# Optimization experiments

Measured on AMD Instinct MI355X. Metric: run time of the kernel, lower is better.

## Reference

```python
import jax, jax.numpy as jnp
import numpy as np

EMBED_DIM = 128
NUM_SYMBOLS = 200000
PAD_IDX = NUM_SYMBOLS
K_NEIGHBORS = 10
PROCESS_STEPS = 4
D_MODEL = 2 * EMBED_DIM   # 256
D_INNER = 2 * D_MODEL     # 512
LSTM_HID = 2 * D_MODEL    # 512
B, F_SUP, MAX_K = 4096, 5, 64


def setup_inputs() -> dict:
    key = jax.random.key(0)
    ks = jax.random.split(key, 40)
    f = lambda i, shape, s=0.05: jax.random.normal(ks[i], shape, jnp.float32) * s
    inp = {}
    inp['query'] = jax.random.randint(ks[0], (B, 2), 0, NUM_SYMBOLS)
    inp['support'] = jax.random.randint(ks[1], (F_SUP, 2), 0, NUM_SYMBOLS)
    inp['q_l1'] = jax.random.randint(ks[2], (B, MAX_K, 2), 0, NUM_SYMBOLS + 1)
    inp['q_deg_l'] = jax.random.randint(ks[3], (B,), 0, 100)
    inp['q_r1'] = jax.random.randint(ks[4], (B, MAX_K, 2), 0, NUM_SYMBOLS + 1)
    inp['q_deg_r'] = jax.random.randint(ks[5], (B,), 0, 100)
    inp['s_l1'] = jax.random.randint(ks[6], (F_SUP, MAX_K, 2), 0, NUM_SYMBOLS + 1)
    inp['s_deg_l'] = jax.random.randint(ks[7], (F_SUP,), 0, 100)
    inp['s_r1'] = jax.random.randint(ks[8], (F_SUP, MAX_K, 2), 0, NUM_SYMBOLS + 1)
    inp['s_deg_r'] = jax.random.randint(ks[9], (F_SUP,), 0, 100)
    # learned parameters
    inp['symbol_emb'] = f(10, (NUM_SYMBOLS + 1, EMBED_DIM), 0.1).at[PAD_IDX].set(0.0)
    inp['gcn_w_w'] = f(11, (EMBED_DIM, 2 * EMBED_DIM))
    inp['gcn_w_b'] = jnp.zeros((EMBED_DIM,), jnp.float32)
    inp['gcn_b'] = jnp.zeros((EMBED_DIM,), jnp.float32)
    inp['g1_w'] = f(12, (EMBED_DIM // 2, EMBED_DIM))
    inp['g1_b'] = jnp.zeros((EMBED_DIM // 2,), jnp.float32)
    inp['ln1_g'] = jnp.ones((EMBED_DIM // 2,), jnp.float32)
    inp['ln1_b'] = jnp.zeros((EMBED_DIM // 2,), jnp.float32)
    inp['g2_w'] = f(13, (1, EMBED_DIM // 2))
    inp['g2_b'] = jnp.zeros((1,), jnp.float32)
    inp['gate_temp'] = jnp.array(1.0, jnp.float32)
    inp['se_p1_w'] = f(14, (D_INNER, D_MODEL))
    inp['se_p1_b'] = jnp.zeros((D_INNER,), jnp.float32)
    inp['se_p2_w'] = f(15, (D_MODEL, D_INNER))
    inp['se_p2_b'] = jnp.zeros((D_MODEL,), jnp.float32)
    inp['se_ln_g'] = jnp.ones((D_MODEL,), jnp.float32)
    inp['se_ln_b'] = jnp.zeros((D_MODEL,), jnp.float32)
    inp['w_ih'] = f(16, (4 * LSTM_HID, D_MODEL))
    inp['w_hh'] = f(17, (4 * LSTM_HID, LSTM_HID))
    inp['b_ih'] = jnp.zeros((4 * LSTM_HID,), jnp.float32)
    inp['b_hh'] = jnp.zeros((4 * LSTM_HID,), jnp.float32)
    return inp


def _layernorm(x, g, b, eps=1e-5):
    m = jnp.mean(x, axis=-1, keepdims=True)
    v = jnp.var(x, axis=-1, keepdims=True)
    return (x - m) / jnp.sqrt(v + eps) * g + b


def _l2norm(x):
    return x / jnp.maximum(jnp.linalg.norm(x, axis=-1, keepdims=True), 1e-12)


def _neighbor_encoder(conn, deg, self_ids, p):
    emb = p['symbol_emb']
    rel, ent = conn[:, :, 0], conn[:, :, 1]
    rel_emb = emb[rel]            # [n, K, D] gather
    ent_emb = emb[ent]            # [n, K, D]
    self_emb = emb[self_ids]      # [n, D]
    sim = jnp.einsum('nd,nkd->nk', _l2norm(self_emb), _l2norm(ent_emb))
    is_pad = (rel == PAD_IDX).astype(jnp.float32)
    sim = sim - is_pad * 1e9
    k = min(K_NEIGHBORS, conn.shape[1])
    _, k_idx = jax.lax.top_k(sim, k)
    bidx = jnp.arange(conn.shape[0])[:, None]
    k_mask = jnp.zeros(sim.shape, jnp.float32).at[bidx, k_idx].set(1.0)[..., None]
    concat = jnp.concatenate([rel_emb, ent_emb], axis=-1)   # [n, K, 2D]
    proj = jax.nn.leaky_relu(concat @ p['gcn_w_w'].T + p['gcn_w_b'] + p['gcn_b'], 0.01)
    valid = (1.0 - is_pad[..., None]) * k_mask
    denom = jnp.maximum(jnp.sum(valid, axis=1), 1.0)
    agg = jnp.sum((proj * k_mask) * valid, axis=1) / denom   # [n, D]
    h = jax.nn.relu(_layernorm(agg @ p['g1_w'].T + p['g1_b'], p['ln1_g'], p['ln1_b']))
    logit = h @ p['g2_w'].T + p['g2_b']                      # [n, 1]
    temp = jnp.clip(p['gate_temp'], 0.1, 5.0)
    gate = jax.nn.sigmoid(logit / temp) * (deg > 0).astype(jnp.float32)[:, None]
    return jnp.tanh(self_emb + gate * agg)


def _support_encoder(x, p):
    h = jax.nn.relu(x @ p['se_p1_w'].T + p['se_p1_b'])
    h = h @ p['se_p2_w'].T + p['se_p2_b']
    return _layernorm(h + x, p['se_ln_g'], p['se_ln_b'])


def _query_encoder(support, query, p):
    n = query.shape[0]
    h_r0 = jnp.zeros((n, LSTM_HID), jnp.float32)
    c0 = jnp.zeros((n, LSTM_HID), jnp.float32)

    def step(carry, _):
        h_r, c = carry
        gates = query @ p['w_ih'].T + p['b_ih'] + h_r @ p['w_hh'].T + p['b_hh']
        i, f, g, o = jnp.split(gates, 4, axis=-1)
        c = jax.nn.sigmoid(f) * c + jax.nn.sigmoid(i) * jnp.tanh(g)
        h_ = jax.nn.sigmoid(o) * jnp.tanh(c)
        h = query + h_[:, :D_MODEL]
        attn = jax.nn.softmax(h @ support.T, axis=1)
        r = attn @ support
        return (jnp.concatenate([h, r], axis=-1), c), None

    (h_r, _), _ = jax.lax.scan(step, (h_r0, c0), None, length=PROCESS_STEPS)
    return h_r[:, :D_MODEL]


def reference(query, support, q_l1, q_deg_l, q_r1, q_deg_r, s_l1, s_deg_l, s_r1, s_deg_r,
              symbol_emb, gcn_w_w, gcn_w_b, gcn_b, g1_w, g1_b, ln1_g, ln1_b, g2_w, g2_b,
              gate_temp, se_p1_w, se_p1_b, se_p2_w, se_p2_b, se_ln_g, se_ln_b,
              w_ih, w_hh, b_ih, b_hh):
    p = dict(symbol_emb=symbol_emb, gcn_w_w=gcn_w_w, gcn_w_b=gcn_w_b, gcn_b=gcn_b,
             g1_w=g1_w, g1_b=g1_b, ln1_g=ln1_g, ln1_b=ln1_b, g2_w=g2_w, g2_b=g2_b,
             gate_temp=gate_temp, se_p1_w=se_p1_w, se_p1_b=se_p1_b, se_p2_w=se_p2_w,
             se_p2_b=se_p2_b, se_ln_g=se_ln_g, se_ln_b=se_ln_b,
             w_ih=w_ih, w_hh=w_hh, b_ih=b_ih, b_hh=b_hh)
    q_left = _neighbor_encoder(q_l1, q_deg_l, query[:, 0], p)
    q_right = _neighbor_encoder(q_r1, q_deg_r, query[:, 1], p)
    query_vec = jnp.concatenate([q_left, q_right], axis=-1)      # [B, 2D]
    s_left = _neighbor_encoder(s_l1, s_deg_l, support[:, 0], p)
    s_right = _neighbor_encoder(s_r1, s_deg_r, support[:, 1], p)
    support_vec = jnp.concatenate([s_left, s_right], axis=-1)    # [F, 2D]
    support_g = jnp.mean(_support_encoder(support_vec, p), axis=0, keepdims=True)  # [1, 2D]
    query_enc = _support_encoder(query_vec, p)                   # [B, 2D]
    query_g = _query_encoder(support_g, query_enc, p)            # [B, 2D]
    return jnp.sum(query_g * support_g, axis=1)                  # [B]
```

## Files before the change

### kernel.cpp

```cpp
#include <hip/hip_runtime.h>
#include <math.h>

#define BQ 4096
#define F_SUP 5
#define MAXK 64
#define ED 128
#define DM 256
#define DI 512
#define LH 512
#define NG 2048
#define PADX 200000
#define KNB 10
#define MROWS 82048
#define MREAL 82020
#define MQ 4224

typedef unsigned short u16;
typedef __attribute__((ext_vector_type(8))) short short8;
typedef __attribute__((ext_vector_type(4))) float floatx4;

__device__ __forceinline__ float sigf(float x) { return 1.0f / (1.0f + __expf(-x)); }
__device__ __forceinline__ float tanh_fast(float x) {
  float a = fabsf(x);
  float e = __expf(-2.0f * a);
  float t = (1.0f - e) / (1.0f + e);
  return copysignf(t, x);
}
__device__ __forceinline__ u16 f2bf(float f) {
  unsigned u = __float_as_uint(f);
  unsigned r = (u + 0x7FFFu + ((u >> 16) & 1u)) >> 16;
  return (u16)r;
}
__device__ __forceinline__ float bf2f(u16 u) {
  return __uint_as_float(((unsigned)u) << 16);
}
__device__ __forceinline__ void gl2lds16(const void* g, void* l) {
  __builtin_amdgcn_global_load_lds(
      (const __attribute__((address_space(1))) void*)g,
      (__attribute__((address_space(3))) void*)l, 16, 0, 0);
}

__global__ __launch_bounds__(256) void nbr_topk_kernel(
    const int* __restrict__ query, const int* __restrict__ support,
    const int* __restrict__ q_l1, const int* __restrict__ q_r1,
    const int* __restrict__ s_l1, const int* __restrict__ s_r1,
    const float* __restrict__ emb,
    int* __restrict__ idxA, int* __restrict__ meta)
{
  __shared__ int relS[64], entS[64];
  __shared__ __align__(16) float sE[128];
  __shared__ float simS[64];
  __shared__ int selS[16];
  __shared__ int cntS;
  __shared__ float nsS;

  int tid = threadIdx.x;
  int b = blockIdx.x;
  const int* conn; int self_id;
  if (b < BQ)              { int i = b;              conn = q_l1 + i*(MAXK*2); self_id = query[2*i];   }
  else if (b < 2*BQ)       { int i = b - BQ;         conn = q_r1 + i*(MAXK*2); self_id = query[2*i+1]; }
  else if (b < 2*BQ+F_SUP) { int i = b - 2*BQ;       conn = s_l1 + i*(MAXK*2); self_id = support[2*i]; }
  else                     { int i = b - 2*BQ-F_SUP; conn = s_r1 + i*(MAXK*2); self_id = support[2*i+1]; }

  if (tid < 128) {
    int v = conn[tid];
    if (tid & 1) entS[tid >> 1] = v; else relS[tid >> 1] = v;
    sE[tid] = emb[(long)self_id * ED + tid];
  }
  __syncthreads();
  if (tid < 64) {
    float v = sE[tid]*sE[tid] + sE[tid+64]*sE[tid+64];
    #pragma unroll
    for (int off = 1; off < 64; off <<= 1) v += __shfl_xor(v, off);
    if (tid == 0) nsS = fmaxf(sqrtf(v), 1e-12f);
  }
  __syncthreads();

  {
    int k = tid >> 2, part = tid & 3;
    const float* er = emb + (long)entS[k] * ED + part * 32;
    const float* sr = &sE[part * 32];
    float dot = 0.f, sq = 0.f;
    #pragma unroll
    for (int j = 0; j < 32; j += 4) {
      float4 e = *(const float4*)(er + j);
      float4 s = *(const float4*)(sr + j);
      dot += e.x*s.x + e.y*s.y + e.z*s.z + e.w*s.w;
      sq  += e.x*e.x + e.y*e.y + e.z*e.z + e.w*e.w;
    }
    dot += __shfl_xor(dot, 1); dot += __shfl_xor(dot, 2);
    sq  += __shfl_xor(sq, 1);  sq  += __shfl_xor(sq, 2);
    if (part == 0) {
      float ne = fmaxf(sqrtf(sq), 1e-12f);
      float sim = dot / (nsS * ne);
      if (relS[k] == PADX) sim -= 1e9f;
      simS[k] = sim;
    }
  }
  __syncthreads();

  if (tid < 64) {
    float mys = simS[tid];
    int rank = 0;
    #pragma unroll
    for (int j = 0; j < 64; ++j) {
      float s = simS[j];
      rank += ((s > mys) || (s == mys && j < tid)) ? 1 : 0;
    }
    bool val = (rank < KNB) && (relS[tid] != PADX);
    unsigned long long vm = __ballot(val ? 1 : 0);
    if (val) {
      int pos = __popcll(vm & ((1ull << tid) - 1ull));
      selS[pos] = tid;
    }
    if (tid == 0) { cntS = __popcll(vm); meta[b] = __popcll(vm); }
  }
  __syncthreads();

  int cnt = cntS;
  long base = (long)b * 10;
  if (tid < 2 * KNB) {
    int kk = tid >> 1, h = tid & 1;
    int id = PADX;
    if (kk < cnt) { int k = selS[kk]; id = h ? entS[k] : relS[k]; }
    idxA[(base + kk) * 2 + h] = id;
  }
  if (b == 0 && tid >= 128 && tid < 128 + 2 * (MROWS - MREAL)) {
    idxA[(long)MREAL * 2 + (tid - 128)] = PADX;
  }
}

__global__ __launch_bounds__(256) void proj_gather_gemm(
    const int* __restrict__ idxA, const float* __restrict__ emb,
    const u16* __restrict__ W, u16* __restrict__ proj)
{
  __shared__ u16 As[128 * 32];
  __shared__ u16 Bs[128 * 32];
  __shared__ int idxS[256];
  int tid = threadIdx.x;
  int bm = blockIdx.x;
  idxS[tid] = idxA[bm * 256 + tid];
  int lane = tid & 63, wave = tid >> 6;
  int wm = (wave & 1) * 64, wn = (wave >> 1) * 64;
  int col = lane & 15, quad = lane >> 4;
  int r = tid >> 1, part = tid & 1;

  floatx4 acc[4][4];
  #pragma unroll
  for (int i = 0; i < 4; ++i)
    #pragma unroll
    for (int j = 0; j < 4; ++j) { floatx4 z = {0.f,0.f,0.f,0.f}; acc[i][j] = z; }
  __syncthreads();

  for (int k0 = 0; k0 < 256; k0 += 32) {
    int half = k0 >> 7, koff = k0 & 127;
    #pragma unroll
    for (int t = 0; t < 2; ++t) {
      int c = t * 256 + tid;
      int rb = c >> 2, o = c & 3;
      int og = o ^ (rb & 3);
      gl2lds16(W + (long)rb * 256 + k0 + og * 8, &Bs[(size_t)c * 8]);
    }
    {
      int id = idxS[r * 2 + half];
      const float* src = emb + (long)id * ED + koff + part * 16;
      float4 f0 = *(const float4*)(src);
      float4 f1 = *(const float4*)(src + 4);
      float4 f2 = *(const float4*)(src + 8);
      float4 f3 = *(const float4*)(src + 12);
      short8 s0, s1;
      s0[0]=(short)f2bf(f0.x); s0[1]=(short)f2bf(f0.y); s0[2]=(short)f2bf(f0.z); s0[3]=(short)f2bf(f0.w);
      s0[4]=(short)f2bf(f1.x); s0[5]=(short)f2bf(f1.y); s0[6]=(short)f2bf(f1.z); s0[7]=(short)f2bf(f1.w);
      s1[0]=(short)f2bf(f2.x); s1[1]=(short)f2bf(f2.y); s1[2]=(short)f2bf(f2.z); s1[3]=(short)f2bf(f2.w);
      s1[4]=(short)f2bf(f3.x); s1[5]=(short)f2bf(f3.y); s1[6]=(short)f2bf(f3.z); s1[7]=(short)f2bf(f3.w);
      int o0 = 2 * part, o1 = 2 * part + 1;
      *(short8*)&As[(size_t)(r * 4 + (o0 ^ (r & 3))) * 8] = s0;
      *(short8*)&As[(size_t)(r * 4 + (o1 ^ (r & 3))) * 8] = s1;
    }
    __syncthreads();
    short8 af[4], bfr[4];
    #pragma unroll
    for (int i = 0; i < 4; ++i) {
      int ra = wm + i * 16 + col;
      af[i] = *(const short8*)&As[(size_t)(ra * 4 + (quad ^ (ra & 3))) * 8];
      int rb = wn + i * 16 + col;
      bfr[i] = *(const short8*)&Bs[(size_t)(rb * 4 + (quad ^ (rb & 3))) * 8];
    }
    #pragma unroll
    for (int i = 0; i < 4; ++i)
      #pragma unroll
      for (int j = 0; j < 4; ++j)
        acc[i][j] = __builtin_amdgcn_mfma_f32_16x16x32_bf16(af[i], bfr[j], acc[i][j], 0, 0, 0);
    __syncthreads();
  }
  int gm0 = bm * 128 + wm + quad * 4;
  int gn0 = wn + col;
  #pragma unroll
  for (int i = 0; i < 4; ++i)
    #pragma unroll
    for (int j = 0; j < 4; ++j)
      #pragma unroll
      for (int rr = 0; rr < 4; ++rr)
        proj[(long)(gm0 + i * 16 + rr) * 128 + gn0 + j * 16] = f2bf(acc[i][j][rr]);
}

__global__ __launch_bounds__(128) void nbr_post_kernel(
    const int* __restrict__ query, const int* __restrict__ support,
    const int* __restrict__ q_deg_l, const int* __restrict__ q_deg_r,
    const int* __restrict__ s_deg_l, const int* __restrict__ s_deg_r,
    const float* __restrict__ emb,
    const u16* __restrict__ proj, const int* __restrict__ meta,
    const float* __restrict__ gcn_w_b, const float* __restrict__ gcn_b,
    const float* __restrict__ g1_w, const float* __restrict__ g1_b,
    const float* __restrict__ ln1_g, const float* __restrict__ ln1_b,
    const float* __restrict__ g2_w, const float* __restrict__ g2_b,
    const float* __restrict__ gate_temp,
    float* __restrict__ qv, u16* __restrict__ qv_bf)
{
  __shared__ __align__(16) float aggS[128];
  __shared__ float sEs[128];
  __shared__ float gateS;
  int tid = threadIdx.x, b = blockIdx.x;
  int deg, self_id, row, colb;
  if (b < BQ)              { int i = b;              deg = q_deg_l[i]; self_id = query[2*i];     row = i;        colb = 0;  }
  else if (b < 2*BQ)       { int i = b - BQ;         deg = q_deg_r[i]; self_id = query[2*i+1];   row = i;        colb = ED; }
  else if (b < 2*BQ+F_SUP) { int i = b - 2*BQ;       deg = s_deg_l[i]; self_id = support[2*i];   row = BQ + i;   colb = 0;  }
  else                     { int i = b - 2*BQ-F_SUP; deg = s_deg_r[i]; self_id = support[2*i+1]; row = BQ + i;   colb = ED; }
  float* outp = qv + (long)row * DM + colb;
  u16*  outpb = qv_bf + (long)row * DM + colb;

  int cnt = meta[b];
  float denom = fmaxf((float)cnt, 1.0f);
  float bsum = gcn_w_b[tid] + gcn_b[tid];
  float agg = 0.f;
  long pbase = (long)b * 10;
  for (int kk = 0; kk < cnt; ++kk) {
    float z = bf2f(proj[(pbase + kk) * 128 + tid]) + bsum;
    z = (z >= 0.f) ? z : 0.01f * z;
    agg += z;
  }
  agg /= denom;
  aggS[tid] = agg;
  sEs[tid] = emb[(long)self_id * ED + tid];
  __syncthreads();

  if (tid < 64) {
    int e = tid;
    const float4* g1r = (const float4*)(g1_w + e * ED);
    float y = g1_b[e];
    #pragma unroll 8
    for (int j = 0; j < 32; ++j) {
      float4 w = g1r[j];
      float4 a = *(const float4*)&aggS[j * 4];
      y += w.x*a.x + w.y*a.y + w.z*a.z + w.w*a.w;
    }
    float s = y;
    #pragma unroll
    for (int off = 1; off < 64; off <<= 1) s += __shfl_xor(s, off);
    float mean = s * (1.0f / 64.0f);
    float dv = y - mean;
    float s2 = dv * dv;
    #pragma unroll
    for (int off = 1; off < 64; off <<= 1) s2 += __shfl_xor(s2, off);
    float var = s2 * (1.0f / 64.0f);
    float hv = dv / sqrtf(var + 1e-5f) * ln1_g[e] + ln1_b[e];
    hv = fmaxf(hv, 0.f);
    float lp = hv * g2_w[e];
    #pragma unroll
    for (int off = 1; off < 64; off <<= 1) lp += __shfl_xor(lp, off);
    if (e == 0) {
      float logit = lp + g2_b[0];
      float temp = fminf(fmaxf(gate_temp[0], 0.1f), 5.0f);
      float gate = 1.0f / (1.0f + expf(-logit / temp));
      if (deg <= 0) gate = 0.f;
      gateS = gate;
    }
  }
  __syncthreads();
  float o = tanhf(sEs[tid] + gateS * aggS[tid]);
  outp[tid] = o;
  outpb[tid] = f2bf(o);
}

__global__ __launch_bounds__(256) void mfma_gemm(
    const u16* __restrict__ A, int lda,
    const u16* __restrict__ W, int ldw,
    int N, int K,
    float* __restrict__ Cout, u16* __restrict__ Cbf,
    const float* __restrict__ bias0,
    const u16* __restrict__ gqin,
    u16* __restrict__ gqout,
    int relu, int lstm_mode,
    float* __restrict__ cstate, const float* __restrict__ qe,
    u16* __restrict__ hbf)
{
  __shared__ u16 As[128 * 32];
  __shared__ u16 Bs[128 * 32];
  int tid = threadIdx.x;
  int nb = N >> 7;
  int bn = blockIdx.x % nb, bm = blockIdx.x / nb;
  int lane = tid & 63, wave = tid >> 6;
  int wm = (wave & 1) * 64, wn = (wave >> 1) * 64;
  int col = lane & 15, quad = lane >> 4;

  u16 gqa[64]; float cpv[16]; float qev[16]; float scv[4];
  int u = 0; long fb = 0;
  if (lstm_mode) {
    u = bn * 32 + (wave >> 1) * 16 + col;
    fb = ((long)blockIdx.x * 4 + wave) * 64 + lane;
    #pragma unroll
    for (int j = 0; j < 4; ++j)
      scv[j] = bias0[bn * 128 + (wave >> 1) * 64 + j * 16 + col];
    if (lstm_mode == 1) {
      const short8* gp = (const short8*)(gqin + fb * 64);
      #pragma unroll
      for (int t = 0; t < 8; ++t) *(short8*)&gqa[t * 8] = gp[t];
      const float4* cp = (const float4*)(cstate + fb * 16);
      #pragma unroll
      for (int t = 0; t < 4; ++t) *(float4*)&cpv[t * 4] = cp[t];
    }
    if (u < DM) {
      #pragma unroll
      for (int i = 0; i < 4; ++i)
        #pragma unroll
        for (int r = 0; r < 4; ++r) {
          int m = bm * 128 + (wave & 1) * 64 + i * 16 + quad * 4 + r;
          qev[i * 4 + r] = qe[(long)m * DM + u];
        }
    }
  }

  floatx4 acc[4][4];
  #pragma unroll
  for (int i = 0; i < 4; ++i)
    #pragma unroll
    for (int j = 0; j < 4; ++j) { floatx4 z = {0.f,0.f,0.f,0.f}; acc[i][j] = z; }

  for (int k0 = 0; k0 < K; k0 += 32) {
    #pragma unroll
    for (int t = 0; t < 2; ++t) {
      int c = t * 256 + tid;
      int r = c >> 2, o = c & 3;
      int og = o ^ (r & 3);
      gl2lds16(A + (long)(bm * 128 + r) * lda + k0 + og * 8, &As[(size_t)c * 8]);
      gl2lds16(W + (long)(bn * 128 + r) * ldw + k0 + og * 8, &Bs[(size_t)c * 8]);
    }
    __syncthreads();
    short8 af[4], bfr[4];
    #pragma unroll
    for (int i = 0; i < 4; ++i) {
      int ra = wm + i * 16 + col;
      af[i] = *(const short8*)&As[(size_t)(ra * 4 + (quad ^ (ra & 3))) * 8];
      int rb = wn + i * 16 + col;
      bfr[i] = *(const short8*)&Bs[(size_t)(rb * 4 + (quad ^ (rb & 3))) * 8];
    }
    #pragma unroll
    for (int i = 0; i < 4; ++i)
      #pragma unroll
      for (int j = 0; j < 4; ++j)
        acc[i][j] = __builtin_amdgcn_mfma_f32_16x16x32_bf16(af[i], bfr[j], acc[i][j], 0, 0, 0);
    __syncthreads();
  }

  if (lstm_mode) {
    float cnew[16];
    #pragma unroll
    for (int i = 0; i < 4; ++i) {
      #pragma unroll
      for (int r = 0; r < 4; ++r) {
        float gI = acc[i][0][r] + scv[0];
        float gF = acc[i][1][r] + scv[1];
        float gG = acc[i][2][r] + scv[2];
        float gO = acc[i][3][r] + scv[3];
        if (lstm_mode == 1) {
          gI += bf2f(gqa[(i * 4 + 0) * 4 + r]);
          gF += bf2f(gqa[(i * 4 + 1) * 4 + r]);
          gG += bf2f(gqa[(i * 4 + 2) * 4 + r]);
          gO += bf2f(gqa[(i * 4 + 3) * 4 + r]);
        }
        float cp = (lstm_mode == 2) ? 0.f : cpv[i * 4 + r];
        float cn = sigf(gF) * cp + sigf(gI) * tanh_fast(gG);
        cnew[i * 4 + r] = cn;
        if (u < DM) {
          int m = bm * 128 + (wave & 1) * 64 + i * 16 + quad * 4 + r;
          hbf[(long)m * DM + u] = f2bf(qev[i * 4 + r] + sigf(gO) * tanh_fast(cn));
        }
      }
    }
    {
      float4* cp = (float4*)(cstate + fb * 16);
      #pragma unroll
      for (int t = 0; t < 4; ++t) cp[t] = *(float4*)&cnew[t * 4];
    }
    if (lstm_mode == 2) {
      u16 ga[64];
      #pragma unroll
      for (int i = 0; i < 4; ++i)
        #pragma unroll
        for (int j = 0; j < 4; ++j)
          #pragma unroll
          for (int r = 0; r < 4; ++r)
            ga[(i * 4 + j) * 4 + r] = f2bf(acc[i][j][r] + scv[j]);
      short8* gp = (short8*)(gqout + fb * 64);
      #pragma unroll
      for (int t = 0; t < 8; ++t) gp[t] = *(short8*)&ga[t * 8];
    }
  } else {
    int gm0 = bm * 128 + wm + quad * 4;
    int gn0 = bn * 128 + wn + col;
    #pragma unroll
    for (int i = 0; i < 4; ++i) {
      #pragma unroll
      for (int j = 0; j < 4; ++j) {
        int n = gn0 + j * 16;
        #pragma unroll
        for (int r = 0; r < 4; ++r) {
          int m = gm0 + i * 16 + r;
          float v = acc[i][j][r];
          if (bias0) v += bias0[n];
          if (relu) v = fmaxf(v, 0.f);
          if (Cout) Cout[(long)m * N + n] = v;
          if (Cbf)  Cbf[(long)m * N + n] = f2bf(v);
        }
      }
    }
  }
}

__global__ void prep_cast(
    const float* __restrict__ p1, const float* __restrict__ p2,
    const float* __restrict__ gcnw, const float* __restrict__ wih,
    const float* __restrict__ whh, const float* __restrict__ bih,
    const float* __restrict__ bhh,
    u16* __restrict__ p1b, u16* __restrict__ p2b, u16* __restrict__ gcnb,
    u16* __restrict__ wihb, u16* __restrict__ whhb, float* __restrict__ bihh)
{
  int gid = blockIdx.x * 256 + threadIdx.x;
  if (gid < 131072) { p1b[gid] = f2bf(p1[gid]); }
  else if (gid < 262144) { int i = gid - 131072; p2b[i] = f2bf(p2[i]); }
  else if (gid < 294912) { int i = gid - 262144; gcnb[i] = f2bf(gcnw[i]); }
  else if (gid < 819200) {
    int i = gid - 294912; int p = i >> 8, k = i & 255;
    int g = (p >> 4) & 3, uu = (p >> 7) * 32 + ((p >> 6) & 1) * 16 + (p & 15);
    int n = g * 512 + uu;
    wihb[i] = f2bf(wih[(long)n * DM + k]);
  } else if (gid < 1343488) {
    int i = gid - 819200; int p = i >> 8, k = i & 255;
    int g = (p >> 4) & 3, uu = (p >> 7) * 32 + ((p >> 6) & 1) * 16 + (p & 15);
    int n = g * 512 + uu;
    whhb[i] = f2bf(whh[(long)n * LH + k]);
  } else if (gid < 1345536) {
    int p = gid - 1343488;
    int g = (p >> 4) & 3, uu = (p >> 7) * 32 + ((p >> 6) & 1) * 16 + (p & 15);
    int n = g * 512 + uu;
    bihh[p] = bih[n] + bhh[n];
  }
}

__global__ __launch_bounds__(256) void ln_residual_kernel(
    const float* __restrict__ h2buf, const float* __restrict__ xbuf,
    const float* __restrict__ lng, const float* __restrict__ lnb,
    float* __restrict__ out, u16* __restrict__ outb)
{
  __shared__ float red[4];
  int r = blockIdx.x, tid = threadIdx.x;
  float v = h2buf[(long)r * DM + tid] + xbuf[(long)r * DM + tid];
  float s = v;
  #pragma unroll
  for (int off = 1; off < 64; off <<= 1) s += __shfl_xor(s, off);
  if ((tid & 63) == 0) red[tid >> 6] = s;
  __syncthreads();
  float mean = (red[0] + red[1] + red[2] + red[3]) * (1.0f / 256.0f);
  __syncthreads();
  float dv = v - mean;
  float s2 = dv * dv;
  #pragma unroll
  for (int off = 1; off < 64; off <<= 1) s2 += __shfl_xor(s2, off);
  if ((tid & 63) == 0) red[tid >> 6] = s2;
  __syncthreads();
  float var = (red[0] + red[1] + red[2] + red[3]) * (1.0f / 256.0f);
  float o = dv / sqrtf(var + 1e-5f) * lng[tid] + lnb[tid];
  out[(long)r * DM + tid] = o;
  outb[(long)r * DM + tid] = f2bf(o);
}

__global__ __launch_bounds__(256) void scorr_kernel(
    const float* __restrict__ qe, const float* __restrict__ whh,
    float* __restrict__ sg, float* __restrict__ s_corr_perm)
{
  __shared__ float sgS[DM];
  int tid = threadIdx.x;
  {
    float v = 0.f;
    #pragma unroll
    for (int r = 0; r < F_SUP; ++r) v += qe[(long)(BQ + r) * DM + tid];
    v *= (1.0f / (float)F_SUP);
    sgS[tid] = v;
    if (blockIdx.x == 0) sg[tid] = v;
  }
  __syncthreads();
  int wave = tid >> 6, lane = tid & 63;
  int n = blockIdx.x * 4 + wave;
  float4 w = *(const float4*)(whh + (long)n * LH + DM + lane * 4);
  float4 s = *(const float4*)&sgS[lane * 4];
  float d = w.x*s.x + w.y*s.y + w.z*s.z + w.w*s.w;
  #pragma unroll
  for (int off = 1; off < 64; off <<= 1) d += __shfl_xor(d, off);
  if (lane == 0) {
    int g = n >> 9, uu = n & 511;
    int p = (uu >> 5) * 128 + ((uu >> 4) & 1) * 64 + g * 16 + (uu & 15);
    s_corr_perm[p] = d;
  }
}

__global__ __launch_bounds__(256) void final_dot_kernel(
    const u16* __restrict__ h, const float* __restrict__ sg, float* __restrict__ out)
{
  __shared__ float red[4];
  int m = blockIdx.x, tid = threadIdx.x;
  float v = bf2f(h[(long)m * DM + tid]) * sg[tid];
  #pragma unroll
  for (int off = 1; off < 64; off <<= 1) v += __shfl_xor(v, off);
  if ((tid & 63) == 0) red[tid >> 6] = v;
  __syncthreads();
  if (tid == 0) out[m] = red[0] + red[1] + red[2] + red[3];
}

extern "C" void kernel_launch(void* const* d_in, const int* in_sizes, int n_in,
                              void* d_out, int out_size, void* d_ws, size_t ws_size,
                              hipStream_t stream)
{
  const int*   query    = (const int*)  d_in[0];
  const int*   support  = (const int*)  d_in[1];
  const int*   q_l1     = (const int*)  d_in[2];
  const int*   q_deg_l  = (const int*)  d_in[3];
  const int*   q_r1     = (const int*)  d_in[4];
  const int*   q_deg_r  = (const int*)  d_in[5];
  const int*   s_l1     = (const int*)  d_in[6];
  const int*   s_deg_l  = (const int*)  d_in[7];
  const int*   s_r1     = (const int*)  d_in[8];
  const int*   s_deg_r  = (const int*)  d_in[9];
  const float* symbol_emb = (const float*)d_in[10];
  const float* gcn_w_w  = (const float*)d_in[11];
  const float* gcn_w_b  = (const float*)d_in[12];
  const float* gcn_b    = (const float*)d_in[13];
  const float* g1_w     = (const float*)d_in[14];
  const float* g1_b     = (const float*)d_in[15];
  const float* ln1_g    = (const float*)d_in[16];
  const float* ln1_b    = (const float*)d_in[17];
  const float* g2_w     = (const float*)d_in[18];
  const float* g2_b     = (const float*)d_in[19];
  const float* gate_temp= (const float*)d_in[20];
  const float* se_p1_w  = (const float*)d_in[21];
  const float* se_p1_b  = (const float*)d_in[22];
  const float* se_p2_w  = (const float*)d_in[23];
  const float* se_p2_b  = (const float*)d_in[24];
  const float* se_ln_g  = (const float*)d_in[25];
  const float* se_ln_b  = (const float*)d_in[26];
  const float* w_ih     = (const float*)d_in[27];
  const float* w_hh     = (const float*)d_in[28];
  const float* b_ih     = (const float*)d_in[29];
  const float* b_hh     = (const float*)d_in[30];

  float* ws = (float*)d_ws;
  size_t off = 0;
  float* projF   = ws + off; off += (size_t)MROWS * 128 / 2;
  float* idxF    = ws + off; off += (size_t)MROWS * 2;
  float* qv      = ws + off; off += (size_t)MQ * DM;
  float* qe      = ws + off; off += (size_t)MQ * DM;
  float* qv_bfF  = ws + off; off += (size_t)MQ * DM / 2;
  float* qe_bfF  = ws + off; off += (size_t)MQ * DM / 2;
  float* h1bF    = ws + off; off += (size_t)MQ * DI / 2;
  float* H2      = ws + off; off += (size_t)MQ * DM;
  float* gqbF    = ws + off; off += (size_t)BQ * NG / 2;
  float* cstate  = ws + off; off += (size_t)BQ * LH;
  float* hbf0F   = ws + off; off += (size_t)BQ * DM / 2;
  float* hbf1F   = ws + off; off += (size_t)BQ * DM / 2;
  float* p1bF    = ws + off; off += 131072 / 2;
  float* p2bF    = ws + off; off += 131072 / 2;
  float* gcnbF   = ws + off; off += 32768 / 2;
  float* wihbF   = ws + off; off += 524288 / 2;
  float* whhbF   = ws + off; off += 524288 / 2;
  float* bihh    = ws + off; off += 2048;
  float* sg      = ws + off; off += 256;
  float* s_corr  = ws + off; off += 2048;
  float* metaF   = ws + off; off += 8448;

  u16* proj   = (u16*)projF;
  int* idxA   = (int*)idxF;
  u16* qv_bf  = (u16*)qv_bfF;
  u16* qe_bf  = (u16*)qe_bfF;
  u16* H1_bf  = (u16*)h1bF;
  u16* gq_fr  = (u16*)gqbF;
  u16* hbf0   = (u16*)hbf0F;
  u16* hbf1   = (u16*)hbf1F;
  u16* p1b    = (u16*)p1bF;
  u16* p2b    = (u16*)p2bF;
  u16* gcnb   = (u16*)gcnbF;
  u16* wihb   = (u16*)wihbF;
  u16* whhb   = (u16*)whhbF;
  int* meta   = (int*)metaF;

  prep_cast<<<5256, 256, 0, stream>>>(se_p1_w, se_p2_w, gcn_w_w, w_ih, w_hh, b_ih, b_hh,
                                      p1b, p2b, gcnb, wihb, whhb, bihh);

  nbr_topk_kernel<<<2 * BQ + 2 * F_SUP, 256, 0, stream>>>(
      query, support, q_l1, q_r1, s_l1, s_r1, symbol_emb, idxA, meta);

  proj_gather_gemm<<<MROWS / 128, 256, 0, stream>>>(idxA, symbol_emb, gcnb, proj);

  nbr_post_kernel<<<2 * BQ + 2 * F_SUP, 128, 0, stream>>>(
      query, support, q_deg_l, q_deg_r, s_deg_l, s_deg_r, symbol_emb,
      proj, meta, gcn_w_b, gcn_b, g1_w, g1_b, ln1_g, ln1_b, g2_w, g2_b, gate_temp,
      qv, qv_bf);

  mfma_gemm<<<(MQ / 128) * (DI / 128), 256, 0, stream>>>(qv_bf, 256, p1b, 256, DI, 256,
      nullptr, H1_bf, se_p1_b, nullptr, nullptr, 1, 0, nullptr, nullptr, nullptr);
  mfma_gemm<<<(MQ / 128) * (DM / 128), 256, 0, stream>>>(H1_bf, 512, p2b, 512, DM, 512,
      H2, nullptr, se_p2_b, nullptr, nullptr, 0, 0, nullptr, nullptr, nullptr);
  ln_residual_kernel<<<BQ + F_SUP, 256, 0, stream>>>(H2, qv, se_ln_g, se_ln_b, qe, qe_bf);

  scorr_kernel<<<512, 256, 0, stream>>>(qe, w_hh, sg, s_corr);

  mfma_gemm<<<(BQ / 128) * (NG / 128), 256, 0, stream>>>(qe_bf, 256, wihb, 256, NG, 256,
      nullptr, nullptr, bihh, nullptr, gq_fr, 0, 2, cstate, qe, hbf0);

  mfma_gemm<<<(BQ / 128) * (NG / 128), 256, 0, stream>>>(hbf0, 256, whhb, 256, NG, 256,
      nullptr, nullptr, s_corr, gq_fr, nullptr, 0, 1, cstate, qe, hbf1);
  mfma_gemm<<<(BQ / 128) * (NG / 128), 256, 0, stream>>>(hbf1, 256, whhb, 256, NG, 256,
      nullptr, nullptr, s_corr, gq_fr, nullptr, 0, 1, cstate, qe, hbf0);
  mfma_gemm<<<(BQ / 128) * (NG / 128), 256, 0, stream>>>(hbf0, 256, whhb, 256, NG, 256,
      nullptr, nullptr, s_corr, gq_fr, nullptr, 0, 1, cstate, qe, hbf1);

  final_dot_kernel<<<BQ, 256, 0, stream>>>(hbf1, sg, (float*)d_out);
}
```

Before: 430.7 us.

## Load MFMA fragments directly from global memory, dropping LDS staging and barriers

Both the gather-projection GEMM and the generic MFMA GEMM stop staging A/B tiles through shared memory. Each wave instead loads its own bf16 fragments from global (or gathers and converts embedding rows) directly into registers, with no __syncthreads. K becomes a template parameter with partial unrolling. This removes LDS traffic and barrier stalls, at the cost of redundant per-wave global loads and less coalesced access, which relies on L1/L2 hits.

```diff
diff --git a/kernel.cpp b/kernel.cpp
--- a/kernel.cpp
+++ b/kernel.cpp
@@ -34,11 +34,6 @@
 __device__ __forceinline__ float bf2f(u16 u) {
   return __uint_as_float(((unsigned)u) << 16);
 }
-__device__ __forceinline__ void gl2lds16(const void* g, void* l) {
-  __builtin_amdgcn_global_load_lds(
-      (const __attribute__((address_space(1))) void*)g,
-      (__attribute__((address_space(3))) void*)l, 16, 0, 0);
-}
 
 __global__ __launch_bounds__(256) void nbr_topk_kernel(
     const int* __restrict__ query, const int* __restrict__ support,
@@ -134,64 +129,50 @@
     const int* __restrict__ idxA, const float* __restrict__ emb,
     const u16* __restrict__ W, u16* __restrict__ proj)
 {
-  __shared__ u16 As[128 * 32];
-  __shared__ u16 Bs[128 * 32];
-  __shared__ int idxS[256];
   int tid = threadIdx.x;
   int bm = blockIdx.x;
-  idxS[tid] = idxA[bm * 256 + tid];
   int lane = tid & 63, wave = tid >> 6;
   int wm = (wave & 1) * 64, wn = (wave >> 1) * 64;
   int col = lane & 15, quad = lane >> 4;
-  int r = tid >> 1, part = tid & 1;
+
+  int ids[4][2];
+  #pragma unroll
+  for (int i = 0; i < 4; ++i) {
+    int row = bm * 128 + wm + i * 16 + col;
+    ids[i][0] = idxA[row * 2];
+    ids[i][1] = idxA[row * 2 + 1];
+  }
+  const u16* Bbase = W + (long)(wn + col) * 256 + quad * 8;
 
   floatx4 acc[4][4];
   #pragma unroll
   for (int i = 0; i < 4; ++i)
     #pragma unroll
     for (int j = 0; j < 4; ++j) { floatx4 z = {0.f,0.f,0.f,0.f}; acc[i][j] = z; }
-  __syncthreads();
-
+
+  #pragma unroll 2
   for (int k0 = 0; k0 < 256; k0 += 32) {
-    int half = k0 >> 7, koff = k0 & 127;
-    #pragma unroll
-    for (int t = 0; t < 2; ++t) {
-      int c = t * 256 + tid;
-      int rb = c >> 2, o = c & 3;
-      int og = o ^ (rb & 3);
-      gl2lds16(W + (long)rb * 256 + k0 + og * 8, &Bs[(size_t)c * 8]);
-    }
-    {
-      int id = idxS[r * 2 + half];
-      const float* src = emb + (long)id * ED + koff + part * 16;
+    int hsel = k0 >> 7;
+    int kk = (k0 & 127) + quad * 8;
+    short8 af[4], bfr[4];
+    #pragma unroll
+    for (int i = 0; i < 4; ++i) {
+      const float* src = emb + (long)ids[i][hsel] * ED + kk;
       float4 f0 = *(const float4*)(src);
       float4 f1 = *(const float4*)(src + 4);
-      float4 f2 = *(const float4*)(src + 8);
-      float4 f3 = *(const float4*)(src + 12);
-      short8 s0, s1;
-      s0[0]=(short)f2bf(f0.x); s0[1]=(short)f2bf(f0.y); s0[2]=(short)f2bf(f0.z); s0[3]=(short)f2bf(f0.w);
-      s0[4]=(short)f2bf(f1.x); s0[5]=(short)f2bf(f1.y); s0[6]=(short)f2bf(f1.z); s0[7]=(short)f2bf(f1.w);
-      s1[0]=(short)f2bf(f2.x); s1[1]=(short)f2bf(f2.y); s1[2]=(short)f2bf(f2.z); s1[3]=(short)f2bf(f2.w);
-      s1[4]=(short)f2bf(f3.x); s1[5]=(short)f2bf(f3.y); s1[6]=(short)f2bf(f3.z); s1[7]=(short)f2bf(f3.w);
-      int o0 = 2 * part, o1 = 2 * part + 1;
-      *(short8*)&As[(size_t)(r * 4 + (o0 ^ (r & 3))) * 8] = s0;
-      *(short8*)&As[(size_t)(r * 4 + (o1 ^ (r & 3))) * 8] = s1;
-    }
-    __syncthreads();
-    short8 af[4], bfr[4];
-    #pragma unroll
-    for (int i = 0; i < 4; ++i) {
-      int ra = wm + i * 16 + col;
-      af[i] = *(const short8*)&As[(size_t)(ra * 4 + (quad ^ (ra & 3))) * 8];
-      int rb = wn + i * 16 + col;
-      bfr[i] = *(const short8*)&Bs[(size_t)(rb * 4 + (quad ^ (rb & 3))) * 8];
-    }
+      short8 s;
+      s[0]=(short)f2bf(f0.x); s[1]=(short)f2bf(f0.y); s[2]=(short)f2bf(f0.z); s[3]=(short)f2bf(f0.w);
+      s[4]=(short)f2bf(f1.x); s[5]=(short)f2bf(f1.y); s[6]=(short)f2bf(f1.z); s[7]=(short)f2bf(f1.w);
+      af[i] = s;
+    }
+    #pragma unroll
+    for (int j = 0; j < 4; ++j)
+      bfr[j] = *(const short8*)(Bbase + (long)j * 16 * 256 + k0);
     #pragma unroll
     for (int i = 0; i < 4; ++i)
       #pragma unroll
       for (int j = 0; j < 4; ++j)
         acc[i][j] = __builtin_amdgcn_mfma_f32_16x16x32_bf16(af[i], bfr[j], acc[i][j], 0, 0, 0);
-    __syncthreads();
   }
   int gm0 = bm * 128 + wm + quad * 4;
   int gn0 = wn + col;
@@ -282,10 +263,11 @@
   outpb[tid] = f2bf(o);
 }
 
+template<int K>
 __global__ __launch_bounds__(256) void mfma_gemm(
     const u16* __restrict__ A, int lda,
     const u16* __restrict__ W, int ldw,
-    int N, int K,
+    int N,
     float* __restrict__ Cout, u16* __restrict__ Cbf,
     const float* __restrict__ bias0,
     const u16* __restrict__ gqin,
@@ -294,8 +276,6 @@
     float* __restrict__ cstate, const float* __restrict__ qe,
     u16* __restrict__ hbf)
 {
-  __shared__ u16 As[128 * 32];
-  __shared__ u16 Bs[128 * 32];
   int tid = threadIdx.x;
   int nb = N >> 7;
   int bn = blockIdx.x % nb, bm = blockIdx.x / nb;
@@ -330,36 +310,29 @@
     }
   }
 
+  const u16* Abase = A + (long)(bm * 128 + wm + col) * lda + quad * 8;
+  const u16* Bbase = W + (long)(bn * 128 + wn + col) * ldw + quad * 8;
+
   floatx4 acc[4][4];
   #pragma unroll
   for (int i = 0; i < 4; ++i)
     #pragma unroll
     for (int j = 0; j < 4; ++j) { floatx4 z = {0.f,0.f,0.f,0.f}; acc[i][j] = z; }
 
+  #pragma unroll 2
   for (int k0 = 0; k0 < K; k0 += 32) {
-    #pragma unroll
-    for (int t = 0; t < 2; ++t) {
-      int c = t * 256 + tid;
-      int r = c >> 2, o = c & 3;
-      int og = o ^ (r & 3);
-      gl2lds16(A + (long)(bm * 128 + r) * lda + k0 + og * 8, &As[(size_t)c * 8]);
-      gl2lds16(W + (long)(bn * 128 + r) * ldw + k0 + og * 8, &Bs[(size_t)c * 8]);
-    }
-    __syncthreads();
     short8 af[4], bfr[4];
     #pragma unroll
-    for (int i = 0; i < 4; ++i) {
-      int ra = wm + i * 16 + col;
-      af[i] = *(const short8*)&As[(size_t)(ra * 4 + (quad ^ (ra & 3))) * 8];
-      int rb = wn + i * 16 + col;
-      bfr[i] = *(const short8*)&Bs[(size_t)(rb * 4 + (quad ^ (rb & 3))) * 8];
-    }
+    for (int i = 0; i < 4; ++i)
+      af[i] = *(const short8*)(Abase + (long)i * 16 * lda + k0);
+    #pragma unroll
+    for (int j = 0; j < 4; ++j)
+      bfr[j] = *(const short8*)(Bbase + (long)j * 16 * ldw + k0);
     #pragma unroll
     for (int i = 0; i < 4; ++i)
       #pragma unroll
       for (int j = 0; j < 4; ++j)
         acc[i][j] = __builtin_amdgcn_mfma_f32_16x16x32_bf16(af[i], bfr[j], acc[i][j], 0, 0, 0);
-    __syncthreads();
   }
 
   if (lstm_mode) {
@@ -614,22 +587,22 @@
       proj, meta, gcn_w_b, gcn_b, g1_w, g1_b, ln1_g, ln1_b, g2_w, g2_b, gate_temp,
       qv, qv_bf);
 
-  mfma_gemm<<<(MQ / 128) * (DI / 128), 256, 0, stream>>>(qv_bf, 256, p1b, 256, DI, 256,
+  mfma_gemm<256><<<(MQ / 128) * (DI / 128), 256, 0, stream>>>(qv_bf, 256, p1b, 256, DI,
       nullptr, H1_bf, se_p1_b, nullptr, nullptr, 1, 0, nullptr, nullptr, nullptr);
-  mfma_gemm<<<(MQ / 128) * (DM / 128), 256, 0, stream>>>(H1_bf, 512, p2b, 512, DM, 512,
+  mfma_gemm<512><<<(MQ / 128) * (DM / 128), 256, 0, stream>>>(H1_bf, 512, p2b, 512, DM,
       H2, nullptr, se_p2_b, nullptr, nullptr, 0, 0, nullptr, nullptr, nullptr);
   ln_residual_kernel<<<BQ + F_SUP, 256, 0, stream>>>(H2, qv, se_ln_g, se_ln_b, qe, qe_bf);
 
   scorr_kernel<<<512, 256, 0, stream>>>(qe, w_hh, sg, s_corr);
 
-  mfma_gemm<<<(BQ / 128) * (NG / 128), 256, 0, stream>>>(qe_bf, 256, wihb, 256, NG, 256,
+  mfma_gemm<256><<<(BQ / 128) * (NG / 128), 256, 0, stream>>>(qe_bf, 256, wihb, 256, NG,
       nullptr, nullptr, bihh, nullptr, gq_fr, 0, 2, cstate, qe, hbf0);
 
-  mfma_gemm<<<(BQ / 128) * (NG / 128), 256, 0, stream>>>(hbf0, 256, whhb, 256, NG, 256,
+  mfma_gemm<256><<<(BQ / 128) * (NG / 128), 256, 0, stream>>>(hbf0, 256, whhb, 256, NG,
       nullptr, nullptr, s_corr, gq_fr, nullptr, 0, 1, cstate, qe, hbf1);
-  mfma_gemm<<<(BQ / 128) * (NG / 128), 256, 0, stream>>>(hbf1, 256, whhb, 256, NG, 256,
+  mfma_gemm<256><<<(BQ / 128) * (NG / 128), 256, 0, stream>>>(hbf1, 256, whhb, 256, NG,
       nullptr, nullptr, s_corr, gq_fr, nullptr, 0, 1, cstate, qe, hbf0);
-  mfma_gemm<<<(BQ / 128) * (NG / 128), 256, 0, stream>>>(hbf0, 256, whhb, 256, NG, 256,
+  mfma_gemm<256><<<(BQ / 128) * (NG / 128), 256, 0, stream>>>(hbf0, 256, whhb, 256, NG,
       nullptr, nullptr, s_corr, gq_fr, nullptr, 0, 1, cstate, qe, hbf1);
 
   final_dot_kernel<<<BQ, 256, 0, stream>>>(hbf1, sg, (float*)d_out);
```

Result: slower. 499.3 us (+15.9%).

## Double-buffer GEMM LDS tiles, store LSTM cell state in bf16, fuse final dot

Applied to the files above, without the earlier changes.

Makes the MFMA GEMM take K as a template parameter and double-buffers the A/B LDS tiles, so the next k-slice is fetched while the current one is multiplied, with one barrier per iteration instead of two. The LSTM cell state is now stored in bf16 instead of fp32, which halves its read and write traffic but adds rounding error. The last LSTM step no longer writes h. It reduces h·support_g inside the GEMM epilogue and atomically adds into the zeroed output, which removes the final_dot kernel. This adds atomics, a memset and LDS usage, and the atomic order makes the result nondeterministic.

```diff
diff --git a/kernel.cpp b/kernel.cpp
--- a/kernel.cpp
+++ b/kernel.cpp
@@ -282,20 +282,23 @@
   outpb[tid] = f2bf(o);
 }
 
+template<int K>
 __global__ __launch_bounds__(256) void mfma_gemm(
     const u16* __restrict__ A, int lda,
     const u16* __restrict__ W, int ldw,
-    int N, int K,
+    int N,
     float* __restrict__ Cout, u16* __restrict__ Cbf,
     const float* __restrict__ bias0,
     const u16* __restrict__ gqin,
     u16* __restrict__ gqout,
     int relu, int lstm_mode,
-    float* __restrict__ cstate, const float* __restrict__ qe,
-    u16* __restrict__ hbf)
-{
-  __shared__ u16 As[128 * 32];
-  __shared__ u16 Bs[128 * 32];
+    u16* __restrict__ cstate, const float* __restrict__ qe,
+    u16* __restrict__ hbf,
+    const float* __restrict__ sgdot, float* __restrict__ dotout)
+{
+  __shared__ u16 As[2][128 * 32];
+  __shared__ u16 Bs[2][128 * 32];
+  __shared__ float dotS[4][4][16];
   int tid = threadIdx.x;
   int nb = N >> 7;
   int bn = blockIdx.x % nb, bm = blockIdx.x / nb;
@@ -303,7 +306,7 @@
   int wm = (wave & 1) * 64, wn = (wave >> 1) * 64;
   int col = lane & 15, quad = lane >> 4;
 
-  u16 gqa[64]; float cpv[16]; float qev[16]; float scv[4];
+  u16 gqa[64]; u16 cpv[16]; float qev[16]; float scv[4]; float sgv = 0.f;
   int u = 0; long fb = 0;
   if (lstm_mode) {
     u = bn * 32 + (wave >> 1) * 16 + col;
@@ -315,11 +318,12 @@
       const short8* gp = (const short8*)(gqin + fb * 64);
       #pragma unroll
       for (int t = 0; t < 8; ++t) *(short8*)&gqa[t * 8] = gp[t];
-      const float4* cp = (const float4*)(cstate + fb * 16);
-      #pragma unroll
-      for (int t = 0; t < 4; ++t) *(float4*)&cpv[t * 4] = cp[t];
+      const short8* cp = (const short8*)(cstate + fb * 16);
+      #pragma unroll
+      for (int t = 0; t < 2; ++t) *(short8*)&cpv[t * 8] = cp[t];
     }
     if (u < DM) {
+      if (sgdot) sgv = sgdot[u];
       #pragma unroll
       for (int i = 0; i < 4; ++i)
         #pragma unroll
@@ -336,34 +340,47 @@
     #pragma unroll
     for (int j = 0; j < 4; ++j) { floatx4 z = {0.f,0.f,0.f,0.f}; acc[i][j] = z; }
 
+  #pragma unroll
+  for (int t = 0; t < 2; ++t) {
+    int c = t * 256 + tid;
+    int r = c >> 2, o = c & 3;
+    int og = o ^ (r & 3);
+    gl2lds16(A + (long)(bm * 128 + r) * lda + 0 + og * 8, &As[0][(size_t)c * 8]);
+    gl2lds16(W + (long)(bn * 128 + r) * ldw + 0 + og * 8, &Bs[0][(size_t)c * 8]);
+  }
+
   for (int k0 = 0; k0 < K; k0 += 32) {
-    #pragma unroll
-    for (int t = 0; t < 2; ++t) {
-      int c = t * 256 + tid;
-      int r = c >> 2, o = c & 3;
-      int og = o ^ (r & 3);
-      gl2lds16(A + (long)(bm * 128 + r) * lda + k0 + og * 8, &As[(size_t)c * 8]);
-      gl2lds16(W + (long)(bn * 128 + r) * ldw + k0 + og * 8, &Bs[(size_t)c * 8]);
-    }
+    int cur = (k0 >> 5) & 1;
     __syncthreads();
+    if (k0 + 32 < K) {
+      int nxt = cur ^ 1;
+      #pragma unroll
+      for (int t = 0; t < 2; ++t) {
+        int c = t * 256 + tid;
+        int r = c >> 2, o = c & 3;
+        int og = o ^ (r & 3);
+        gl2lds16(A + (long)(bm * 128 + r) * lda + (k0 + 32) + og * 8, &As[nxt][(size_t)c * 8]);
+        gl2lds16(W + (long)(bn * 128 + r) * ldw + (k0 + 32) + og * 8, &Bs[nxt][(size_t)c * 8]);
+      }
+    }
     short8 af[4], bfr[4];
     #pragma unroll
     for (int i = 0; i < 4; ++i) {
       int ra = wm + i * 16 + col;
-      af[i] = *(const short8*)&As[(size_t)(ra * 4 + (quad ^ (ra & 3))) * 8];
+      af[i] = *(const short8*)&As[cur][(size_t)(ra * 4 + (quad ^ (ra & 3))) * 8];
       int rb = wn + i * 16 + col;
-      bfr[i] = *(const short8*)&Bs[(size_t)(rb * 4 + (quad ^ (rb & 3))) * 8];
+      bfr[i] = *(const short8*)&Bs[cur][(size_t)(rb * 4 + (quad ^ (rb & 3))) * 8];
     }
     #pragma unroll
     for (int i = 0; i < 4; ++i)
       #pragma unroll
       for (int j = 0; j < 4; ++j)
         acc[i][j] = __builtin_amdgcn_mfma_f32_16x16x32_bf16(af[i], bfr[j], acc[i][j], 0, 0, 0);
-    __syncthreads();
   }
 
   if (lstm_mode) {
-    float cnew[16];
+    u16 cnew[16];
+    float dsum[16];
     #pragma unroll
     for (int i = 0; i < 4; ++i) {
       #pragma unroll
@@ -378,19 +395,22 @@
           gG += bf2f(gqa[(i * 4 + 2) * 4 + r]);
           gO += bf2f(gqa[(i * 4 + 3) * 4 + r]);
         }
-        float cp = (lstm_mode == 2) ? 0.f : cpv[i * 4 + r];
+        float cp = (lstm_mode == 2) ? 0.f : bf2f(cpv[i * 4 + r]);
         float cn = sigf(gF) * cp + sigf(gI) * tanh_fast(gG);
-        cnew[i * 4 + r] = cn;
-        if (u < DM) {
+        cnew[i * 4 + r] = f2bf(cn);
+        float hv = 0.f;
+        if (u < DM) hv = qev[i * 4 + r] + sigf(gO) * tanh_fast(cn);
+        if (sgdot) dsum[i * 4 + r] = hv * sgv;
+        else if (u < DM) {
           int m = bm * 128 + (wave & 1) * 64 + i * 16 + quad * 4 + r;
-          hbf[(long)m * DM + u] = f2bf(qev[i * 4 + r] + sigf(gO) * tanh_fast(cn));
+          hbf[(long)m * DM + u] = f2bf(hv);
         }
       }
     }
-    {
-      float4* cp = (float4*)(cstate + fb * 16);
-      #pragma unroll
-      for (int t = 0; t < 4; ++t) cp[t] = *(float4*)&cnew[t * 4];
+    if (!sgdot || bn * 32 < DM) {
+      short8* cp = (short8*)(cstate + fb * 16);
+      #pragma unroll
+      for (int t = 0; t < 2; ++t) cp[t] = *(short8*)&cnew[t * 8];
     }
     if (lstm_mode == 2) {
       u16 ga[64];
@@ -404,6 +424,30 @@
       short8* gp = (short8*)(gqout + fb * 64);
       #pragma unroll
       for (int t = 0; t < 8; ++t) gp[t] = *(short8*)&ga[t * 8];
+    }
+    if (sgdot && bn < (DM / 32)) {
+      #pragma unroll
+      for (int t = 0; t < 16; ++t) {
+        float v = dsum[t];
+        v += __shfl_xor(v, 1);
+        v += __shfl_xor(v, 2);
+        v += __shfl_xor(v, 4);
+        v += __shfl_xor(v, 8);
+        dsum[t] = v;
+      }
+      if (col == 0) {
+        #pragma unroll
+        for (int t = 0; t < 16; ++t) dotS[wave][quad][t] = dsum[t];
+      }
+      __syncthreads();
+      if (tid < 128) {
+        int m = tid;
+        int h = (m >= 64) ? 1 : 0;
+        int q = (m >> 2) & 3;
+        int idx = ((m & 63) >> 4) * 4 + (m & 3);
+        float v = dotS[h][q][idx] + dotS[h + 2][q][idx];
+        atomicAdd(dotout + bm * 128 + m, v);
+      }
     }
   } else {
     int gm0 = bm * 128 + wm + quad * 4;
@@ -511,19 +555,6 @@
     int p = (uu >> 5) * 128 + ((uu >> 4) & 1) * 64 + g * 16 + (uu & 15);
     s_corr_perm[p] = d;
   }
-}
-
-__global__ __launch_bounds__(256) void final_dot_kernel(
-    const u16* __restrict__ h, const float* __restrict__ sg, float* __restrict__ out)
-{
-  __shared__ float red[4];
-  int m = blockIdx.x, tid = threadIdx.x;
-  float v = bf2f(h[(long)m * DM + tid]) * sg[tid];
-  #pragma unroll
-  for (int off = 1; off < 64; off <<= 1) v += __shfl_xor(v, off);
-  if ((tid & 63) == 0) red[tid >> 6] = v;
-  __syncthreads();
-  if (tid == 0) out[m] = red[0] + red[1] + red[2] + red[3];
 }
 
 extern "C" void kernel_launch(void* const* d_in, const int* in_sizes, int n_in,
@@ -573,7 +604,7 @@
   float* h1bF    = ws + off; off += (size_t)MQ * DI / 2;
   float* H2      = ws + off; off += (size_t)MQ * DM;
   float* gqbF    = ws + off; off += (size_t)BQ * NG / 2;
-  float* cstate  = ws + off; off += (size_t)BQ * LH;
+  float* cstateF = ws + off; off += (size_t)BQ * LH / 2;
   float* hbf0F   = ws + off; off += (size_t)BQ * DM / 2;
   float* hbf1F   = ws + off; off += (size_t)BQ * DM / 2;
   float* p1bF    = ws + off; off += 131072 / 2;
@@ -592,6 +623,7 @@
   u16* qe_bf  = (u16*)qe_bfF;
   u16* H1_bf  = (u16*)h1bF;
   u16* gq_fr  = (u16*)gqbF;
+  u16* cstate = (u16*)cstateF;
   u16* hbf0   = (u16*)hbf0F;
   u16* hbf1   = (u16*)hbf1F;
   u16* p1b    = (u16*)p1bF;
@@ -600,6 +632,9 @@
   u16* wihb   = (u16*)wihbF;
   u16* whhb   = (u16*)whhbF;
   int* meta   = (int*)metaF;
+  float* outF = (float*)d_out;
+
+  hipMemsetAsync(d_out, 0, (size_t)out_size * sizeof(float), stream);
 
   prep_cast<<<5256, 256, 0, stream>>>(se_p1_w, se_p2_w, gcn_w_w, w_ih, w_hh, b_ih, b_hh,
                                       p1b, p2b, gcnb, wihb, whhb, bihh);
@@ -614,23 +649,22 @@
       proj, meta, gcn_w_b, gcn_b, g1_w, g1_b, ln1_g, ln1_b, g2_w, g2_b, gate_temp,
       qv, qv_bf);
 
-  mfma_gemm<<<(MQ / 128) * (DI / 128), 256, 0, stream>>>(qv_bf, 256, p1b, 256, DI, 256,
-      nullptr, H1_bf, se_p1_b, nullptr, nullptr, 1, 0, nullptr, nullptr, nullptr);
-  mfma_gemm<<<(MQ / 128) * (DM / 128), 256, 0, stream>>>(H1_bf, 512, p2b, 512, DM, 512,
-      H2, nullptr, se_p2_b, nullptr, nullptr, 0, 0, nullptr, nullptr, nullptr);
+  mfma_gemm<256><<<(MQ / 128) * (DI / 128), 256, 0, stream>>>(qv_bf, 256, p1b, 256, DI,
+      nullptr, H1_bf, se_p1_b, nullptr, nullptr, 1, 0, nullptr, nullptr, nullptr, nullptr, nullptr);
+  mfma_gemm<512><<<(MQ / 128) * (DM / 128), 256, 0, stream>>>(H1_bf, 512, p2b, 512, DM,
+      H2, nullptr, se_p2_b, nullptr, nullptr, 0, 0, nullptr, nullptr, nullptr, nullptr, nullptr);
   ln_residual_kernel<<<BQ + F_SUP, 256, 0, stream>>>(H2, qv, se_ln_g, se_ln_b, qe, qe_bf);
 
   scorr_kernel<<<512, 256, 0, stream>>>(qe, w_hh, sg, s_corr);
 
-  mfma_gemm<<<(BQ / 128) * (NG / 128), 256, 0, stream>>>(qe_bf, 256, wihb, 256, NG, 256,
-      nullptr, nullptr, bihh, nullptr, gq_fr, 0, 2, cstate, qe, hbf0);
-
-  mfma_gemm<<<(BQ / 128) * (NG / 128), 256, 0, stream>>>(hbf0, 256, whhb, 256, NG, 256,
-      nullptr, nullptr, s_corr, gq_fr, nullptr, 0, 1, cstate, qe, hbf1);
-  mfma_gemm<<<(BQ / 128) * (NG / 128), 256, 0, stream>>>(hbf1, 256, whhb, 256, NG, 256,
-      nullptr, nullptr, s_corr, gq_fr, nullptr, 0, 1, cstate, qe, hbf0);
-  mfma_gemm<<<(BQ / 128) * (NG / 128), 256, 0, stream>>>(hbf0, 256, whhb, 256, NG, 256,
-      nullptr, nullptr, s_corr, gq_fr, nullptr, 0, 1, cstate, qe, hbf1);
-
-  final_dot_kernel<<<BQ, 256, 0, stream>>>(hbf1, sg, (float*)d_out);
-}
+  mfma_gemm<256><<<(BQ / 128) * (NG / 128), 256, 0, stream>>>(qe_bf, 256, wihb, 256, NG,
+      nullptr, nullptr, bihh, nullptr, gq_fr, 0, 2, cstate, qe, hbf0, nullptr, nullptr);
+
+  mfma_gemm<256><<<(BQ / 128) * (NG / 128), 256, 0, stream>>>(hbf0, 256, whhb, 256, NG,
+      nullptr, nullptr, s_corr, gq_fr, nullptr, 0, 1, cstate, qe, hbf1, nullptr, nullptr);
+  mfma_gemm<256><<<(BQ / 128) * (NG / 128), 256, 0, stream>>>(hbf1, 256, whhb, 256, NG,
+      nullptr, nullptr, s_corr, gq_fr, nullptr, 0, 1, cstate, qe, hbf0, nullptr, nullptr);
+
+  mfma_gemm<256><<<(BQ / 128) * (NG / 128), 256, 0, stream>>>(hbf0, 256, whhb, 256, NG,
+      nullptr, nullptr, s_corr, gq_fr, nullptr, 0, 1, cstate, qe, nullptr, sg, outF);
+}
```

After: 451.5 us. 4.8% more time.
